# Optimization experiments

Hardware: AMD Instinct MI355X
Metric: run time of the kernel (lower is better)

Reference implementation:

```python
import jax, jax.numpy as jnp
import numpy as np

N, IN, OUT, T = 65536, 256, 256, 8


def setup_inputs() -> dict:
    key = jax.random.key(0)
    k1, k2, k3, k4 = jax.random.split(key, 4)
    x = jax.random.normal(k1, (N, IN), dtype=jnp.float32)
    types = jax.random.randint(k2, (N,), 0, T, dtype=jnp.int32)
    # xavier_uniform for W: limit = sqrt(6 / (fan_in + fan_out)) with fan computed
    # on the last two dims (out_size, in_size)
    limit = float(np.sqrt(6.0 / (IN + OUT)))
    W = jax.random.uniform(k3, (T, OUT, IN), dtype=jnp.float32, minval=-limit, maxval=limit)
    # original inits b to zeros; use small random values so the bias path is exercised
    b = 0.01 * jax.random.normal(k4, (T, OUT), dtype=jnp.float32)
    return {"x": x, "types": types, "W": W, "b": b}


def reference(x, types, W, b):
    # out[i] = W[types[i]] @ x[i] + b[types[i]]
    # Grouped-GEMM expressed as a loop over the small fixed set of types,
    # avoiding the huge [N, OUT, IN] gather of W[types].
    num_types = W.shape[0]
    out = b[types]  # [N, OUT]
    for t in range(num_types):
        mask = (types == t)[:, None]  # [N, 1]
        out = out + jnp.where(mask, x @ W[t].T, jnp.float32(0.0))
    return out
```

## Files before the change

### kernel.cpp

```cpp
#include <hip/hip_runtime.h>
#include <hip/hip_bf16.h>
#include <stdint.h>


#define NROWS 65536
#define NTYPES 8
#define KDIM 256
#define ODIM 256
#define BM 128
#define BN 128
#define BK 64

typedef __attribute__((ext_vector_type(8))) short short8;
typedef __attribute__((ext_vector_type(4))) float f32x4;

__device__ __forceinline__ unsigned short f2bf(float f) {
    unsigned int u = __float_as_uint(f);
    u += 0x7fffu + ((u >> 16) & 1u);
    return (unsigned short)(u >> 16);
}

__global__ void prep_kernel(const float* __restrict__ W,
                            unsigned short* __restrict__ Wb,
                            int* __restrict__ cnt) {
    if (blockIdx.x == 0 && threadIdx.x < NTYPES) cnt[threadIdx.x] = 0;
    int i = blockIdx.x * 256 + threadIdx.x;
    float4 v = ((const float4*)W)[i];
    ushort4 p;
    p.x = f2bf(v.x); p.y = f2bf(v.y); p.z = f2bf(v.z); p.w = f2bf(v.w);
    ((ushort4*)Wb)[i] = p;
}

__global__ void bucket_kernel(const int* __restrict__ types,
                              int* __restrict__ cnt,
                              int* __restrict__ idx) {
    __shared__ int h[NTYPES];
    __shared__ int base[NTYPES];
    int i = blockIdx.x * 256 + threadIdx.x;
    if (threadIdx.x < NTYPES) h[threadIdx.x] = 0;
    __syncthreads();
    int t = types[i];
    int r = atomicAdd(&h[t], 1);
    __syncthreads();
    if (threadIdx.x < NTYPES)
        base[threadIdx.x] = atomicAdd(&cnt[threadIdx.x], h[threadIdx.x]);
    __syncthreads();
    idx[t * NROWS + base[t] + r] = i;
}

__global__ __launch_bounds__(256, 2)
void gemm_kernel(const float* __restrict__ x,
                 const float* __restrict__ bias,
                 const unsigned short* __restrict__ Wb,
                 const int* __restrict__ cnt,
                 const int* __restrict__ idx,
                 float* __restrict__ out) {
    const int t = blockIdx.z;
    const int count = cnt[t];
    const int m0 = blockIdx.x * BM;
    if (m0 >= count) return;
    const int n0 = blockIdx.y * BN;

    __shared__ int idx_s[BM];
    __shared__ float bias_s[BN];
    __shared__ unsigned short As[BM * BK];
    __shared__ unsigned short Bs[BN * BK];

    const int tid = threadIdx.x;

    if (tid < BM) {
        int m = m0 + tid;
        idx_s[tid] = (m < count) ? idx[t * NROWS + m] : 0;
    } else {
        bias_s[tid - BM] = bias[t * ODIM + n0 + (tid - BM)];
    }
    __syncthreads();

    const int wave = tid >> 6;
    const int lane = tid & 63;
    const int lr = lane & 15;
    const int lq = lane >> 4;
    const int wm = (wave >> 1) * 64;
    const int wn = (wave & 1) * 64;

    f32x4 acc[4][4] = {};

    const int srow = tid >> 4;
    const int sc   = tid & 15;

    char* AsB = (char*)As;
    char* BsB = (char*)Bs;

    for (int k0 = 0; k0 < KDIM; k0 += BK) {
        #pragma unroll
        for (int j = 0; j < 8; ++j) {
            int row = j * 16 + srow;
            const float4 v = *(const float4*)(x + (size_t)idx_s[row] * KDIM + k0 + sc * 4);
            ushort4 p;
            p.x = f2bf(v.x); p.y = f2bf(v.y); p.z = f2bf(v.z); p.w = f2bf(v.w);
            int ch = (sc >> 1) ^ (row & 7);
            *(ushort4*)(AsB + row * 128 + ch * 16 + (sc & 1) * 8) = p;
        }
        #pragma unroll
        for (int it = 0; it < 4; ++it) {
            int dbyte = wave * 4096 + it * 1024;
            int drow  = (dbyte >> 7) + (lane >> 3);
            int schunk = (lane & 7) ^ (lane >> 3);
            const unsigned short* src =
                Wb + (size_t)(t * ODIM + n0 + drow) * KDIM + k0 + schunk * 8;
            __builtin_amdgcn_global_load_lds(
                (const __attribute__((address_space(1))) void*)src,
                (__attribute__((address_space(3))) void*)(BsB + dbyte),
                16, 0, 0);
        }
        __syncthreads();

        #pragma unroll
        for (int kh = 0; kh < 2; ++kh) {
            short8 af[4], bf[4];
            #pragma unroll
            for (int i = 0; i < 4; ++i) {
                int arow = wm + i * 16 + lr;
                int ach = ((kh << 2) + lq) ^ (arow & 7);
                af[i] = *(const short8*)(AsB + arow * 128 + ach * 16);
            }
            #pragma unroll
            for (int i = 0; i < 4; ++i) {
                int brow = wn + i * 16 + lr;
                int bch = ((kh << 2) + lq) ^ (brow & 7);
                bf[i] = *(const short8*)(BsB + brow * 128 + bch * 16);
            }
            #pragma unroll
            for (int i = 0; i < 4; ++i)
                #pragma unroll
                for (int j = 0; j < 4; ++j)
                    acc[i][j] = __builtin_amdgcn_mfma_f32_16x16x32_bf16(
                        af[i], bf[j], acc[i][j], 0, 0, 0);
        }
        __syncthreads();
    }

    #pragma unroll
    for (int i = 0; i < 4; ++i) {
        int lmBase = wm + i * 16 + lq * 4;
        #pragma unroll
        for (int r = 0; r < 4; ++r) {
            int lm = lmBase + r;
            if (m0 + lm < count) {
                size_t orow = (size_t)idx_s[lm] * ODIM;
                #pragma unroll
                for (int j = 0; j < 4; ++j) {
                    int col = wn + j * 16 + lr;
                    out[orow + n0 + col] = acc[i][j][r] + bias_s[col];
                }
            }
        }
    }
}

extern "C" void kernel_launch(void* const* d_in, const int* in_sizes, int n_in,
                              void* d_out, int out_size, void* d_ws, size_t ws_size,
                              hipStream_t stream) {
    const float* x     = (const float*)d_in[0];
    const int*   types = (const int*)d_in[1];
    const float* W     = (const float*)d_in[2];
    const float* b     = (const float*)d_in[3];
    float* out = (float*)d_out;

    char* ws = (char*)d_ws;
    int* cnt = (int*)ws;
    int* idx = (int*)(ws + 1024);
    unsigned short* Wb = (unsigned short*)(ws + 1024 + (size_t)NTYPES * NROWS * sizeof(int));

    prep_kernel<<<512, 256, 0, stream>>>(W, Wb, cnt);
    bucket_kernel<<<NROWS / 256, 256, 0, stream>>>(types, cnt, idx);
    dim3 grid(NROWS / BM, ODIM / BN, NTYPES);
    gemm_kernel<<<grid, 256, 0, stream>>>(x, b, Wb, cnt, idx, out);
}
```

Baseline: 143.3 us.

## Compact tile list, deterministic bucketing, and double-buffer the grouped GEMM K-loop

The old single bucketing pass is replaced by three passes: a per-block histogram fused with the W-to-bf16 conversion, a scan that builds a compact list of (type, row offset) tiles, and a deterministic scatter. The GEMM grid now launches only about 544 tile slots instead of 512×8 mostly-empty blocks that exit early. The GEMM K loop is double-buffered, so the next W tile (loaded straight into LDS) and the next x rows (held in registers) are fetched while the current tile's MFMAs run. This adds one extra small kernel launch and a single-block scan, and doubles the LDS used for staging, which may limit occupancy.

```diff
diff --git a/kernel.cpp b/kernel.cpp
--- a/kernel.cpp
+++ b/kernel.cpp
@@ -10,6 +10,8 @@
 #define BM 128
 #define BN 128
 #define BK 64
+#define HB 64
+#define MAXTILES 544
 
 typedef __attribute__((ext_vector_type(8))) short short8;
 typedef __attribute__((ext_vector_type(4))) float f32x4;
@@ -20,62 +22,100 @@
     return (unsigned short)(u >> 16);
 }
 
-__global__ void prep_kernel(const float* __restrict__ W,
-                            unsigned short* __restrict__ Wb,
-                            int* __restrict__ cnt) {
-    if (blockIdx.x == 0 && threadIdx.x < NTYPES) cnt[threadIdx.x] = 0;
-    int i = blockIdx.x * 256 + threadIdx.x;
-    float4 v = ((const float4*)W)[i];
-    ushort4 p;
-    p.x = f2bf(v.x); p.y = f2bf(v.y); p.z = f2bf(v.z); p.w = f2bf(v.w);
-    ((ushort4*)Wb)[i] = p;
-}
-
-__global__ void bucket_kernel(const int* __restrict__ types,
-                              int* __restrict__ cnt,
-                              int* __restrict__ idx) {
+__global__ void prep_hist_kernel(const int* __restrict__ types,
+                                 const float* __restrict__ W,
+                                 unsigned short* __restrict__ Wb,
+                                 int* __restrict__ blockHist) {
+    __shared__ int h[NTYPES];
+    const int tid = threadIdx.x;
+    if (tid < NTYPES) h[tid] = 0;
+    __syncthreads();
+    const int i = blockIdx.x * 1024 + tid;
+    atomicAdd(&h[types[i]], 1);
+    #pragma unroll
+    for (int r = 0; r < 2; ++r) {
+        int j = i + r * 65536;
+        float4 v = ((const float4*)W)[j];
+        ushort4 p;
+        p.x = f2bf(v.x); p.y = f2bf(v.y); p.z = f2bf(v.z); p.w = f2bf(v.w);
+        ((ushort4*)Wb)[j] = p;
+    }
+    __syncthreads();
+    if (tid < NTYPES) blockHist[blockIdx.x * NTYPES + tid] = h[tid];
+}
+
+__global__ void scan_kernel(const int* __restrict__ blockHist,
+                            int* __restrict__ blockBase,
+                            int* __restrict__ typeBase,
+                            int4* __restrict__ tiles,
+                            int* __restrict__ tileCount) {
+    __shared__ int scnt[NTYPES], sTypeBase[NTYPES], sTileBase[NTYPES + 1];
+    const int tid = threadIdx.x;
+    if (tid < NTYPES) {
+        int run = 0;
+        for (int b = 0; b < HB; ++b) {
+            blockBase[b * NTYPES + tid] = run;
+            run += blockHist[b * NTYPES + tid];
+        }
+        scnt[tid] = run;
+    }
+    __syncthreads();
+    if (tid == 0) {
+        int rowacc = 0, tileacc = 0;
+        for (int t = 0; t < NTYPES; ++t) {
+            sTypeBase[t] = rowacc; typeBase[t] = rowacc; rowacc += scnt[t];
+            sTileBase[t] = tileacc; tileacc += (scnt[t] + BM - 1) / BM;
+        }
+        sTileBase[NTYPES] = tileacc;
+        tileCount[0] = tileacc;
+    }
+    __syncthreads();
+    const int tc = sTileBase[NTYPES];
+    for (int j = tid; j < MAXTILES; j += 64) {
+        if (j < tc) {
+            int t = 0;
+            while (t < NTYPES - 1 && j >= sTileBase[t + 1]) ++t;
+            tiles[j] = make_int4(t, (j - sTileBase[t]) * BM, sTypeBase[t], scnt[t]);
+        }
+    }
+}
+
+__global__ void scatter_kernel(const int* __restrict__ types,
+                               const int* __restrict__ blockBase,
+                               const int* __restrict__ typeBase,
+                               int* __restrict__ idx) {
     __shared__ int h[NTYPES];
     __shared__ int base[NTYPES];
-    int i = blockIdx.x * 256 + threadIdx.x;
-    if (threadIdx.x < NTYPES) h[threadIdx.x] = 0;
-    __syncthreads();
-    int t = types[i];
+    const int tid = threadIdx.x;
+    if (tid < NTYPES) {
+        h[tid] = 0;
+        base[tid] = typeBase[tid] + blockBase[blockIdx.x * NTYPES + tid];
+    }
+    __syncthreads();
+    const int i = blockIdx.x * 1024 + tid;
+    const int t = types[i];
     int r = atomicAdd(&h[t], 1);
-    __syncthreads();
-    if (threadIdx.x < NTYPES)
-        base[threadIdx.x] = atomicAdd(&cnt[threadIdx.x], h[threadIdx.x]);
-    __syncthreads();
-    idx[t * NROWS + base[t] + r] = i;
+    idx[base[t] + r] = i;
 }
 
 __global__ __launch_bounds__(256, 2)
 void gemm_kernel(const float* __restrict__ x,
                  const float* __restrict__ bias,
                  const unsigned short* __restrict__ Wb,
-                 const int* __restrict__ cnt,
+                 const int* __restrict__ tileCount,
+                 const int4* __restrict__ tiles,
                  const int* __restrict__ idx,
                  float* __restrict__ out) {
-    const int t = blockIdx.z;
-    const int count = cnt[t];
-    const int m0 = blockIdx.x * BM;
-    if (m0 >= count) return;
+    if ((int)blockIdx.x >= tileCount[0]) return;
+    const int4 td = tiles[blockIdx.x];
+    const int t = td.x, m0 = td.y, rbase = td.z, count = td.w;
     const int n0 = blockIdx.y * BN;
-
-    __shared__ int idx_s[BM];
-    __shared__ float bias_s[BN];
-    __shared__ unsigned short As[BM * BK];
-    __shared__ unsigned short Bs[BN * BK];
-
-    const int tid = threadIdx.x;
-
-    if (tid < BM) {
-        int m = m0 + tid;
-        idx_s[tid] = (m < count) ? idx[t * NROWS + m] : 0;
-    } else {
-        bias_s[tid - BM] = bias[t * ODIM + n0 + (tid - BM)];
-    }
-    __syncthreads();
-
+    const int rem = count - m0;
+
+    __shared__ unsigned short As[2][BM * BK];
+    __shared__ unsigned short Bs[2][BN * BK];
+
+    const int tid = threadIdx.x;
     const int wave = tid >> 6;
     const int lane = tid & 63;
     const int lr = lane & 15;
@@ -83,79 +123,116 @@
     const int wm = (wave >> 1) * 64;
     const int wn = (wave & 1) * 64;
 
+    const int* rowIdx = idx + rbase + m0;
+
+    const int srow = tid >> 4;
+    const int sc = tid & 15;
+    const float* aptr[8];
+    #pragma unroll
+    for (int j = 0; j < 8; ++j) {
+        int m = j * 16 + srow;
+        aptr[j] = x + (size_t)rowIdx[m < rem ? m : 0] * KDIM + sc * 4;
+    }
+
+    float breg[4];
+    #pragma unroll
+    for (int j = 0; j < 4; ++j) breg[j] = bias[t * ODIM + n0 + wn + j * 16 + lr];
+
+    const int bschunk = (lane & 7) ^ (lane >> 3);
+    const unsigned short* bsrc0 = Wb + (size_t)t * ODIM * KDIM + (size_t)bschunk * 8;
+
     f32x4 acc[4][4] = {};
-
-    const int srow = tid >> 4;
-    const int sc   = tid & 15;
-
-    char* AsB = (char*)As;
-    char* BsB = (char*)Bs;
-
-    for (int k0 = 0; k0 < KDIM; k0 += BK) {
-        #pragma unroll
-        for (int j = 0; j < 8; ++j) {
-            int row = j * 16 + srow;
-            const float4 v = *(const float4*)(x + (size_t)idx_s[row] * KDIM + k0 + sc * 4);
-            ushort4 p;
-            p.x = f2bf(v.x); p.y = f2bf(v.y); p.z = f2bf(v.z); p.w = f2bf(v.w);
-            int ch = (sc >> 1) ^ (row & 7);
-            *(ushort4*)(AsB + row * 128 + ch * 16 + (sc & 1) * 8) = p;
-        }
-        #pragma unroll
-        for (int it = 0; it < 4; ++it) {
-            int dbyte = wave * 4096 + it * 1024;
-            int drow  = (dbyte >> 7) + (lane >> 3);
-            int schunk = (lane & 7) ^ (lane >> 3);
-            const unsigned short* src =
-                Wb + (size_t)(t * ODIM + n0 + drow) * KDIM + k0 + schunk * 8;
-            __builtin_amdgcn_global_load_lds(
-                (const __attribute__((address_space(1))) void*)src,
-                (__attribute__((address_space(3))) void*)(BsB + dbyte),
-                16, 0, 0);
-        }
-        __syncthreads();
-
+    float4 av[8];
+
+#define ISSUE_B(buf, k0)                                                        \
+    {                                                                           \
+        _Pragma("unroll")                                                       \
+        for (int it = 0; it < 4; ++it) {                                        \
+            int dbyte = wave * 4096 + it * 1024;                                \
+            int row = (dbyte >> 7) + (lane >> 3);                               \
+            const unsigned short* src = bsrc0 + (size_t)(n0 + row) * KDIM + (k0); \
+            __builtin_amdgcn_global_load_lds(                                   \
+                (const __attribute__((address_space(1))) void*)src,             \
+                (__attribute__((address_space(3))) void*)((char*)Bs[buf] + dbyte), \
+                16, 0, 0);                                                      \
+        }                                                                       \
+    }
+
+#define LOAD_A(k0)                                                              \
+    {                                                                           \
+        _Pragma("unroll")                                                       \
+        for (int j = 0; j < 8; ++j) av[j] = *(const float4*)(aptr[j] + (k0));   \
+    }
+
+#define WRITE_A(buf)                                                            \
+    {                                                                           \
+        _Pragma("unroll")                                                       \
+        for (int j = 0; j < 8; ++j) {                                           \
+            int row = j * 16 + srow;                                            \
+            ushort4 p;                                                          \
+            p.x = f2bf(av[j].x); p.y = f2bf(av[j].y);                           \
+            p.z = f2bf(av[j].z); p.w = f2bf(av[j].w);                           \
+            int ch = (sc >> 1) ^ (row & 7);                                     \
+            *(ushort4*)((char*)As[buf] + row * 128 + ch * 16 + (sc & 1) * 8) = p; \
+        }                                                                       \
+    }
+
+    ISSUE_B(0, 0);
+    LOAD_A(0);
+    WRITE_A(0);
+    __syncthreads();
+
+    #pragma unroll
+    for (int i = 0; i < 4; ++i) {
+        const int cur = i & 1;
+        if (i < 3) {
+            ISSUE_B(cur ^ 1, (i + 1) * BK);
+            LOAD_A((i + 1) * BK);
+        }
         #pragma unroll
         for (int kh = 0; kh < 2; ++kh) {
-            short8 af[4], bf[4];
+            short8 af[4], bfr[4];
             #pragma unroll
-            for (int i = 0; i < 4; ++i) {
-                int arow = wm + i * 16 + lr;
+            for (int q = 0; q < 4; ++q) {
+                int arow = wm + q * 16 + lr;
                 int ach = ((kh << 2) + lq) ^ (arow & 7);
-                af[i] = *(const short8*)(AsB + arow * 128 + ach * 16);
+                af[q] = *(const short8*)((char*)As[cur] + arow * 128 + ach * 16);
             }
             #pragma unroll
-            for (int i = 0; i < 4; ++i) {
-                int brow = wn + i * 16 + lr;
+            for (int q = 0; q < 4; ++q) {
+                int brow = wn + q * 16 + lr;
                 int bch = ((kh << 2) + lq) ^ (brow & 7);
-                bf[i] = *(const short8*)(BsB + brow * 128 + bch * 16);
+                bfr[q] = *(const short8*)((char*)Bs[cur] + brow * 128 + bch * 16);
             }
             #pragma unroll
-            for (int i = 0; i < 4; ++i)
+            for (int q = 0; q < 4; ++q)
                 #pragma unroll
                 for (int j = 0; j < 4; ++j)
-                    acc[i][j] = __builtin_amdgcn_mfma_f32_16x16x32_bf16(
-                        af[i], bf[j], acc[i][j], 0, 0, 0);
-        }
-        __syncthreads();
-    }
-
-    #pragma unroll
-    for (int i = 0; i < 4; ++i) {
-        int lmBase = wm + i * 16 + lq * 4;
+                    acc[q][j] = __builtin_amdgcn_mfma_f32_16x16x32_bf16(
+                        af[q], bfr[j], acc[q][j], 0, 0, 0);
+        }
+        if (i < 3) {
+            WRITE_A(cur ^ 1);
+            __syncthreads();
+        }
+    }
+
+    #pragma unroll
+    for (int q = 0; q < 4; ++q) {
         #pragma unroll
         for (int r = 0; r < 4; ++r) {
-            int lm = lmBase + r;
-            if (m0 + lm < count) {
-                size_t orow = (size_t)idx_s[lm] * ODIM;
+            int lm = wm + q * 16 + lq * 4 + r;
+            if (lm < rem) {
+                size_t orow = (size_t)rowIdx[lm] * ODIM + n0;
                 #pragma unroll
-                for (int j = 0; j < 4; ++j) {
-                    int col = wn + j * 16 + lr;
-                    out[orow + n0 + col] = acc[i][j][r] + bias_s[col];
-                }
+                for (int j = 0; j < 4; ++j)
+                    out[orow + wn + j * 16 + lr] = acc[q][j][r] + breg[j];
             }
         }
     }
+#undef ISSUE_B
+#undef LOAD_A
+#undef WRITE_A
 }
 
 extern "C" void kernel_launch(void* const* d_in, const int* in_sizes, int n_in,
@@ -168,12 +245,16 @@
     float* out = (float*)d_out;
 
     char* ws = (char*)d_ws;
-    int* cnt = (int*)ws;
-    int* idx = (int*)(ws + 1024);
-    unsigned short* Wb = (unsigned short*)(ws + 1024 + (size_t)NTYPES * NROWS * sizeof(int));
-
-    prep_kernel<<<512, 256, 0, stream>>>(W, Wb, cnt);
-    bucket_kernel<<<NROWS / 256, 256, 0, stream>>>(types, cnt, idx);
-    dim3 grid(NROWS / BM, ODIM / BN, NTYPES);
-    gemm_kernel<<<grid, 256, 0, stream>>>(x, b, Wb, cnt, idx, out);
-}
+    int*  tileCount = (int*)ws;
+    int*  typeBase  = (int*)(ws + 128);
+    int*  blockHist = (int*)(ws + 512);
+    int*  blockBase = (int*)(ws + 2560);
+    int4* tiles     = (int4*)(ws + 4608);
+    int*  idx       = (int*)(ws + 16384);
+    unsigned short* Wb = (unsigned short*)(ws + 278528);
+
+    prep_hist_kernel<<<HB, 1024, 0, stream>>>(types, W, Wb, blockHist);
+    scan_kernel<<<1, 64, 0, stream>>>(blockHist, blockBase, typeBase, tiles, tileCount);
+    scatter_kernel<<<HB, 1024, 0, stream>>>(types, blockBase, typeBase, idx);
+    gemm_kernel<<<dim3(MAXTILES, 2), 256, 0, stream>>>(x, b, Wb, tileCount, tiles, idx, out);
+}
```

New measurement: 144.6 us. No clear change (+0.9%).
